# Kernel optimization log

Hardware: AMD Instinct MI355X
Metric: run time of the kernel (lower is better)

Reference implementation:

```python
import jax, jax.numpy as jnp
import numpy as np
import math

B, T, D = 4, 4096, 1024
N, L = 256, 768
H = 16
TE = 1024  # time_embed_dim


def _ln(x, g, b, eps=1e-5):
    mu = jnp.mean(x, axis=-1, keepdims=True)
    var = jnp.var(x, axis=-1, keepdims=True)
    return (x - mu) * jax.lax.rsqrt(var + eps) * g + b


def setup_inputs() -> dict:
    key = jax.random.key(0)
    ks = jax.random.split(key, 12)
    s = lambda fan_in: 1.0 / math.sqrt(fan_in)
    return {
        "x":   jax.random.normal(ks[0], (B, T, D), jnp.float32),
        "xf":  jax.random.normal(ks[1], (B, N, L), jnp.float32),
        "emb": jax.random.normal(ks[2], (B, TE), jnp.float32),
        # LayerNorm params
        "norm_g": jnp.ones((D,), jnp.float32), "norm_b": jnp.zeros((D,), jnp.float32),
        "tnorm_g": jnp.ones((L,), jnp.float32), "tnorm_b": jnp.zeros((L,), jnp.float32),
        # Q/K/V projections
        "Wq": jax.random.uniform(ks[3], (D, D), jnp.float32, -s(D), s(D)),
        "bq": jnp.zeros((D,), jnp.float32),
        "Wk": jax.random.uniform(ks[4], (L, D), jnp.float32, -s(L), s(L)),
        "bk": jnp.zeros((D,), jnp.float32),
        "Wv": jax.random.uniform(ks[5], (L, D), jnp.float32, -s(L), s(L)),
        "bv": jnp.zeros((D,), jnp.float32),
        # StylizationBlock: emb_layers Linear(TE, 2D)
        "We": jax.random.uniform(ks[6], (TE, 2 * D), jnp.float32, -s(TE), s(TE)),
        "be": jnp.zeros((2 * D,), jnp.float32),
        # StylizationBlock: inner LayerNorm + out Linear(D, D)
        "snorm_g": jnp.ones((D,), jnp.float32), "snorm_b": jnp.zeros((D,), jnp.float32),
        "Wo": jax.random.uniform(ks[7], (D, D), jnp.float32, -s(D), s(D)),
        "bo": jnp.zeros((D,), jnp.float32),
    }


def reference(x, xf, emb, norm_g, norm_b, tnorm_g, tnorm_b,
              Wq, bq, Wk, bk, Wv, bv, We, be, snorm_g, snorm_b, Wo, bo):
    dh = D // H
    xf_n = _ln(xf, tnorm_g, tnorm_b)                      # B,N,L (shared by K and V)
    q = (_ln(x, norm_g, norm_b) @ Wq + bq).reshape(B, T, H, dh)
    k = (xf_n @ Wk + bk).reshape(B, N, H, dh)
    v = (xf_n @ Wv + bv).reshape(B, N, H, dh)
    attn = jnp.einsum('bthd,bnhd->btnh', q, k) / math.sqrt(dh)
    w = jax.nn.softmax(attn, axis=2)                      # softmax over text tokens n
    y = jnp.einsum('btnh,bnhd->bthd', w, v).reshape(B, T, D)
    # StylizationBlock (AdaLN-style)
    emb_out = jax.nn.silu(emb) @ We + be                  # B, 2D
    scale, shift = jnp.split(emb_out[:, None, :], 2, axis=2)
    h = _ln(y, snorm_g, snorm_b) * (1.0 + scale) + shift
    h = jax.nn.silu(h) @ Wo + bo
    return x + h
```

## Files before the change

### kernel.cpp

```cpp
#include <hip/hip_runtime.h>

typedef unsigned short u16;
typedef short bf16x8 __attribute__((ext_vector_type(8)));
typedef float f32x4 __attribute__((ext_vector_type(4)));


__device__ __forceinline__ float b2f(u16 u) {
  union { unsigned int u; float f; } x; x.u = ((unsigned int)u) << 16; return x.f;
}
__device__ __forceinline__ u16 f2b(float f) {
  union { float f; unsigned int u; } x; x.f = f;
  unsigned int u = x.u;
  return (u16)((u + 0x7FFFu + ((u >> 16) & 1u)) >> 16);
}

#define GLOAD_LDS16(g, l)                                                      \
  __builtin_amdgcn_global_load_lds(                                            \
      (const __attribute__((address_space(1))) unsigned int*)(g),              \
      (__attribute__((address_space(3))) unsigned int*)(l), 16, 0, 0)

__global__ __launch_bounds__(256) void transpose4_k(
    const float* __restrict__ Wq, const float* __restrict__ Wk,
    const float* __restrict__ Wv, const float* __restrict__ Wo,
    u16* __restrict__ wqt, u16* __restrict__ wkt,
    u16* __restrict__ wvt, u16* __restrict__ wot,
    float* __restrict__ embo) {
  if (blockIdx.z == 0 && blockIdx.y == 0) {
    int idx = blockIdx.x * 256 + threadIdx.y * 32 + threadIdx.x;
    embo[idx] = 0.f;
  }
  const float* src; u16* dst; int R;
  switch (blockIdx.z) {
    case 0: src = Wq; dst = wqt; R = 1024; break;
    case 1: src = Wk; dst = wkt; R = 768;  break;
    case 2: src = Wv; dst = wvt; R = 768;  break;
    default: src = Wo; dst = wot; R = 1024; break;
  }
  int bx = blockIdx.x * 32, by = blockIdx.y * 32;
  if (by >= R) return;
  __shared__ float t[32][33];
  int x = threadIdx.x, y = threadIdx.y;
#pragma unroll
  for (int i = 0; i < 4; ++i)
    t[y * 4 + i][x] = src[(size_t)(by + y * 4 + i) * 1024 + bx + x];
  __syncthreads();
#pragma unroll
  for (int i = 0; i < 4; ++i)
    dst[(size_t)(bx + y * 4 + i) * R + by + x] = f2b(t[x][y * 4 + i]);
}

__global__ __launch_bounds__(256) void ln_k(const float* __restrict__ in,
                                            const float* __restrict__ g,
                                            const float* __restrict__ bta,
                                            u16* __restrict__ out, int C) {
  int row = blockIdx.x, tid = threadIdx.x;
  const float* p = in + (size_t)row * C;
  int i0 = tid * 4;
  bool act = i0 < C;
  float v0 = 0.f, v1 = 0.f, v2 = 0.f, v3 = 0.f;
  if (act) {
    float4 u = *(const float4*)(p + i0);
    v0 = u.x; v1 = u.y; v2 = u.z; v3 = u.w;
  }
  float s = v0 + v1 + v2 + v3;
  float q = v0 * v0 + v1 * v1 + v2 * v2 + v3 * v3;
  __shared__ float red[8];
#pragma unroll
  for (int m = 32; m; m >>= 1) { s += __shfl_xor(s, m); q += __shfl_xor(q, m); }
  if ((tid & 63) == 0) { red[tid >> 6] = s; red[4 + (tid >> 6)] = q; }
  __syncthreads();
  s = red[0] + red[1] + red[2] + red[3];
  q = red[4] + red[5] + red[6] + red[7];
  float invC = 1.0f / (float)C;
  float mu = s * invC;
  float rs = rsqrtf(q * invC - mu * mu + 1e-5f);
  if (act) {
    float4 ug = *(const float4*)(g + i0);
    float4 ub = *(const float4*)(bta + i0);
    ushort4 o;
    o.x = f2b((v0 - mu) * rs * ug.x + ub.x);
    o.y = f2b((v1 - mu) * rs * ug.y + ub.y);
    o.z = f2b((v2 - mu) * rs * ug.z + ub.z);
    o.w = f2b((v3 - mu) * rs * ug.w + ub.w);
    *(ushort4*)(out + (size_t)row * C + i0) = o;
  }
}

__global__ __launch_bounds__(256) void style_k(const u16* __restrict__ y,
                                               const float* __restrict__ g,
                                               const float* __restrict__ bta,
                                               const float* __restrict__ embo,
                                               u16* __restrict__ out) {
  int row = blockIdx.x, tid = threadIdx.x;
  int b = row >> 12;
  const u16* p = y + (size_t)row * 1024;
  int i0 = tid * 4;
  ushort4 u = *(const ushort4*)(p + i0);
  float v0 = b2f(u.x), v1 = b2f(u.y), v2 = b2f(u.z), v3 = b2f(u.w);
  float s = v0 + v1 + v2 + v3;
  float q = v0 * v0 + v1 * v1 + v2 * v2 + v3 * v3;
  __shared__ float red[8];
#pragma unroll
  for (int m = 32; m; m >>= 1) { s += __shfl_xor(s, m); q += __shfl_xor(q, m); }
  if ((tid & 63) == 0) { red[tid >> 6] = s; red[4 + (tid >> 6)] = q; }
  __syncthreads();
  s = red[0] + red[1] + red[2] + red[3];
  q = red[4] + red[5] + red[6] + red[7];
  const float invC = 1.0f / 1024.0f;
  float mu = s * invC;
  float rs = rsqrtf(q * invC - mu * mu + 1e-5f);
  float4 ug = *(const float4*)(g + i0);
  float4 ub = *(const float4*)(bta + i0);
  float4 sc = *(const float4*)(embo + b * 2048 + i0);
  float4 sh = *(const float4*)(embo + b * 2048 + 1024 + i0);
  float h0 = ((v0 - mu) * rs * ug.x + ub.x) * (1.0f + sc.x) + sh.x;
  float h1 = ((v1 - mu) * rs * ug.y + ub.y) * (1.0f + sc.y) + sh.y;
  float h2 = ((v2 - mu) * rs * ug.z + ub.z) * (1.0f + sc.z) + sh.z;
  float h3 = ((v3 - mu) * rs * ug.w + ub.w) * (1.0f + sc.w) + sh.w;
  ushort4 o;
  o.x = f2b(h0 / (1.0f + __expf(-h0)));
  o.y = f2b(h1 / (1.0f + __expf(-h1)));
  o.z = f2b(h2 / (1.0f + __expf(-h2)));
  o.w = f2b(h3 / (1.0f + __expf(-h3)));
  *(ushort4*)(out + (size_t)row * 1024 + i0) = o;
}

__global__ __launch_bounds__(256) void emb_k(const float* __restrict__ emb,
                                             const float* __restrict__ We,
                                             const float* __restrict__ be,
                                             float* __restrict__ embo) {
  int b = blockIdx.y, tid = threadIdx.x;
  int j = blockIdx.x * 256 + tid;
  int i0 = blockIdx.z * 128;
  __shared__ float se[128];
  if (tid < 128) {
    float v = emb[b * 1024 + i0 + tid];
    se[tid] = v / (1.0f + __expf(-v));
  }
  __syncthreads();
  float acc = (blockIdx.z == 0) ? be[j] : 0.f;
#pragma unroll 8
  for (int i = 0; i < 128; ++i) acc += se[i] * We[(size_t)(i0 + i) * 2048 + j];
  atomicAdd(&embo[b * 2048 + j], acc);
}

__global__ __launch_bounds__(256) void gemm_bt_k(const u16* __restrict__ A,
                                                 const u16* __restrict__ Bt,
                                                 const float* __restrict__ bias,
                                                 const float* __restrict__ res,
                                                 u16* __restrict__ Cb,
                                                 float* __restrict__ Cf,
                                                 int M, int Nn, int K, int mode) {
  __shared__ __align__(16) short As[128 * 64];
  __shared__ __align__(16) short Bs[128 * 64];
  int tid = threadIdx.x;
  int m0 = blockIdx.x * 128, n0 = blockIdx.y * 128;
  int wave = tid >> 6, lane = tid & 63;
  int l16 = lane & 15, quad = lane >> 4;
  int wm = (wave >> 1) * 64, wn = (wave & 1) * 64;

  f32x4 acc[4][4];
#pragma unroll
  for (int i = 0; i < 4; ++i)
#pragma unroll
    for (int j = 0; j < 4; ++j)
#pragma unroll
      for (int r = 0; r < 4; ++r) acc[i][j][r] = 0.f;

  for (int kt = 0; kt < K; kt += 64) {
#pragma unroll
    for (int p = 0; p < 4; ++p) {
      int c = p * 256 + tid;
      int r = c >> 3;
      int cd = ((c & 7) ^ (r & 7)) * 8;
      int lb = (p * 256 + wave * 64) * 8;
      GLOAD_LDS16(A + (size_t)(m0 + r) * K + kt + cd, As + lb);
      GLOAD_LDS16(Bt + (size_t)(n0 + r) * K + kt + cd, Bs + lb);
    }
    __syncthreads();
#pragma unroll
    for (int ks = 0; ks < 2; ++ks) {
      int swz = ((ks * 4 + quad) ^ (l16 & 7)) * 8;
      bf16x8 af[4], bfr[4];
#pragma unroll
      for (int i = 0; i < 4; ++i)
        af[i] = *(const bf16x8*)&As[(wm + i * 16 + l16) * 64 + swz];
#pragma unroll
      for (int j = 0; j < 4; ++j)
        bfr[j] = *(const bf16x8*)&Bs[(wn + j * 16 + l16) * 64 + swz];
#pragma unroll
      for (int i = 0; i < 4; ++i)
#pragma unroll
        for (int j = 0; j < 4; ++j)
          acc[i][j] = __builtin_amdgcn_mfma_f32_16x16x32_bf16(af[i], bfr[j], acc[i][j], 0, 0, 0);
    }
    __syncthreads();
  }

#pragma unroll
  for (int j = 0; j < 4; ++j) {
    int col = n0 + wn + j * 16 + l16;
    float bv = bias[col];
#pragma unroll
    for (int i = 0; i < 4; ++i) {
      int row0 = m0 + wm + i * 16 + quad * 4;
#pragma unroll
      for (int r = 0; r < 4; ++r) {
        int row = row0 + r;
        float v = acc[i][j][r] + bv;
        if (mode == 2) {
          Cf[(size_t)row * Nn + col] = v + res[(size_t)row * Nn + col];
        } else if (mode == 1) {
          Cb[((size_t)((row >> 8) * 1024 + col)) * 256 + (row & 255)] = f2b(v);
        } else {
          Cb[(size_t)row * Nn + col] = f2b(v);
        }
      }
    }
  }
}

__global__ __launch_bounds__(512, 4) void gemm256_k(const u16* __restrict__ A,
                                                    const u16* __restrict__ Bt,
                                                    const float* __restrict__ bias,
                                                    const float* __restrict__ res,
                                                    u16* __restrict__ Cb,
                                                    float* __restrict__ Cf,
                                                    int M, int Nn, int K, int mode) {
  __shared__ __align__(16) short smem[36864];
  short* AsB = smem;
  short* BsB = smem + 12288;
  int tid = threadIdx.x;
  int m0 = blockIdx.x * 128, n0 = blockIdx.y * 256;
  int wave = tid >> 6, lane = tid & 63;
  int l16 = lane & 15, quad = lane >> 4;
  int wm = (wave >> 2) * 64;
  int wn = (wave & 3) * 64;

  size_t offA;
  {
    int r = tid >> 2;
    int cg = (tid & 3) ^ ((r >> 1) & 3);
    offA = (size_t)(m0 + r) * K + cg * 8;
  }
  int ldsA = tid * 8;
  size_t offB[2];
  int ldsB[2];
#pragma unroll
  for (int p = 0; p < 2; ++p) {
    int c = p * 512 + tid;
    int r = c >> 2;
    int cg = (c & 3) ^ ((r >> 1) & 3);
    offB[p] = (size_t)(n0 + r) * K + cg * 8;
    ldsB[p] = c * 8;
  }

  int aoff[4], boff[4];
#pragma unroll
  for (int mi = 0; mi < 4; ++mi) {
    int R = wm + mi * 16 + l16;
    aoff[mi] = R * 32 + ((quad ^ ((R >> 1) & 3)) * 8);
  }
#pragma unroll
  for (int ni = 0; ni < 4; ++ni) {
    int R = wn + ni * 16 + l16;
    boff[ni] = R * 32 + ((quad ^ ((R >> 1) & 3)) * 8);
  }

  f32x4 acc[4][4];
#pragma unroll
  for (int i = 0; i < 4; ++i)
#pragma unroll
    for (int j = 0; j < 4; ++j)
#pragma unroll
      for (int r = 0; r < 4; ++r) acc[i][j][r] = 0.f;

#define STAGE(tt, bufc)                                                        \
  do {                                                                         \
    int kt_ = (tt) * 32;                                                       \
    GLOAD_LDS16(A + offA + kt_, AsB + (bufc) * 4096 + ldsA);                   \
    GLOAD_LDS16(Bt + offB[0] + kt_, BsB + (bufc) * 8192 + ldsB[0]);            \
    GLOAD_LDS16(Bt + offB[1] + kt_, BsB + (bufc) * 8192 + ldsB[1]);            \
  } while (0)

#define COMPUTE(curc)                                                          \
  do {                                                                         \
    const short* as_ = AsB + (curc) * 4096;                                    \
    const short* bs_ = BsB + (curc) * 8192;                                    \
    bf16x8 af[4], bfv[4];                                                      \
    _Pragma("unroll") for (int mi = 0; mi < 4; ++mi)                           \
        af[mi] = *(const bf16x8*)&as_[aoff[mi]];                               \
    _Pragma("unroll") for (int ni = 0; ni < 4; ++ni)                           \
        bfv[ni] = *(const bf16x8*)&bs_[boff[ni]];                              \
    __builtin_amdgcn_s_setprio(1);                                             \
    _Pragma("unroll") for (int mi = 0; mi < 4; ++mi)                           \
      _Pragma("unroll") for (int ni = 0; ni < 4; ++ni)                         \
        acc[mi][ni] = __builtin_amdgcn_mfma_f32_16x16x32_bf16(                 \
            af[mi], bfv[ni], acc[mi][ni], 0, 0, 0);                            \
    __builtin_amdgcn_s_setprio(0);                                             \
  } while (0)

  const int NT = K >> 5;
  STAGE(0, 0);
  STAGE(1, 1);

  int cur = 0;
  for (int t = 0; t < NT - 1; ++t) {
    asm volatile("s_waitcnt vmcnt(3)" ::: "memory");
    __builtin_amdgcn_s_barrier();
    asm volatile("" ::: "memory");
    if (t + 2 < NT) {
      int nb = cur + 2; if (nb >= 3) nb -= 3;
      STAGE(t + 2, nb);
    }
    COMPUTE(cur);
    cur = (cur == 2) ? 0 : cur + 1;
  }
  asm volatile("s_waitcnt vmcnt(0)" ::: "memory");
  __builtin_amdgcn_s_barrier();
  asm volatile("" ::: "memory");
  COMPUTE(cur);
#undef COMPUTE
#undef STAGE

  float* eps = (float*)smem;
  float bv[4];
#pragma unroll
  for (int ni = 0; ni < 4; ++ni) bv[ni] = bias[n0 + wn + ni * 16 + l16];

#pragma unroll
  for (int half = 0; half < 2; ++half) {
    __syncthreads();
    if ((wave >> 2) == half) {
#pragma unroll
      for (int mi = 0; mi < 4; ++mi) {
#pragma unroll
        for (int ni = 0; ni < 4; ++ni) {
          int col = wn + ni * 16 + l16;
#pragma unroll
          for (int r = 0; r < 4; ++r) {
            int row = mi * 16 + quad * 4 + r;
            eps[row * 256 + (col ^ (((row >> 2) & 3) << 3))] =
                acc[mi][ni][r] + bv[ni];
          }
        }
      }
    }
    __syncthreads();
#pragma unroll
    for (int p = 0; p < 8; ++p) {
      int row = wave * 8 + p;
      int grow = m0 + half * 64 + row;
      int colb = (lane * 4) ^ (((row >> 2) & 3) << 3);
      f32x4 v = *(const f32x4*)&eps[row * 256 + colb];
      if (mode == 2) {
        float4 rv = ((const float4*)&res[(size_t)grow * Nn + n0])[lane];
        float4 o;
        o.x = v[0] + rv.x; o.y = v[1] + rv.y;
        o.z = v[2] + rv.z; o.w = v[3] + rv.w;
        ((float4*)&Cf[(size_t)grow * Nn + n0])[lane] = o;
      } else {
        ushort4 o;
        o.x = f2b(v[0]); o.y = f2b(v[1]); o.z = f2b(v[2]); o.w = f2b(v[3]);
        ((ushort4*)&Cb[(size_t)grow * Nn + n0])[lane] = o;
      }
    }
  }
}

__global__ __launch_bounds__(256) void attn_k(const u16* __restrict__ Q,
                                              const u16* __restrict__ Kt,
                                              const u16* __restrict__ VT,
                                              u16* __restrict__ Y) {
  __shared__ __align__(16) short KsPs[256 * 64];
  __shared__ __align__(16) short Vt[64 * 256];
  int tid = threadIdx.x;
  int t0 = blockIdx.x * 64, h = blockIdx.y, b = blockIdx.z;
  int wave = tid >> 6, lane = tid & 63;
  int l16 = lane & 15, quad = lane >> 4;
  int wb = wave * 16;

#pragma unroll
  for (int p = 0; p < 8; ++p) {
    int c = tid + p * 256;
    int n = c >> 3, cd = c & 7;
    *(int4*)&KsPs[n * 64 + ((cd ^ (n & 7)) * 8)] =
        *(const int4*)(Kt + ((size_t)(b * 256 + n)) * 1024 + h * 64 + cd * 8);
  }
#pragma unroll
  for (int p = 0; p < 8; ++p) {
    int c = tid + p * 256;
    int d = c >> 5, ch = c & 31;
    *(int4*)&Vt[d * 256 + ((ch ^ (d & 7)) * 8)] =
        *(const int4*)(VT + ((size_t)(b * 1024 + h * 64 + d)) * 256 + ch * 8);
  }
  const u16* qrow = Q + ((size_t)(b * 4096 + t0 + wb + l16)) * 1024 + h * 64;
  bf16x8 qf0 = *(const bf16x8*)(qrow + quad * 8);
  bf16x8 qf1 = *(const bf16x8*)(qrow + 32 + quad * 8);
  __syncthreads();

  f32x4 sa[16];
#pragma unroll
  for (int mt = 0; mt < 16; ++mt)
#pragma unroll
    for (int r = 0; r < 4; ++r) sa[mt][r] = 0.f;
#pragma unroll
  for (int ks = 0; ks < 2; ++ks) {
    bf16x8 qb = ks ? qf1 : qf0;
#pragma unroll
    for (int mt = 0; mt < 16; ++mt) {
      int n = mt * 16 + l16;
      bf16x8 kf = *(const bf16x8*)&KsPs[n * 64 + (((ks * 4 + quad) ^ (n & 7)) * 8)];
      sa[mt] = __builtin_amdgcn_mfma_f32_16x16x32_bf16(kf, qb, sa[mt], 0, 0, 0);
    }
  }
  __syncthreads();

  const float CLG = 0.18033688011112042f;
  float mx = -3.0e38f;
#pragma unroll
  for (int mt = 0; mt < 16; ++mt)
#pragma unroll
    for (int r = 0; r < 4; ++r) mx = fmaxf(mx, sa[mt][r]);
  mx = fmaxf(mx, __shfl_xor(mx, 16));
  mx = fmaxf(mx, __shfl_xor(mx, 32));
  float mxc = mx * CLG;
  float sum = 0.f;
#pragma unroll
  for (int mt = 0; mt < 16; ++mt)
#pragma unroll
    for (int r = 0; r < 4; ++r) {
      float e = __builtin_exp2f(sa[mt][r] * CLG - mxc);
      sa[mt][r] = e;
      sum += e;
    }
  sum += __shfl_xor(sum, 16);
  sum += __shfl_xor(sum, 32);
  float rsc = 1.0f / sum;

  {
    int prow = wb + l16;
    short* pb = &KsPs[prow * 256 + (quad & 1) * 4];
    int q2 = quad >> 1, swz = l16 & 7;
#pragma unroll
    for (int mt = 0; mt < 16; ++mt) {
      float a0 = sa[mt][0], a1 = sa[mt][1], a2 = sa[mt][2], a3 = sa[mt][3];
      unsigned plo, phi;
      asm("v_cvt_pk_bf16_f32 %0, %1, %2" : "=v"(plo) : "v"(a0), "v"(a1));
      asm("v_cvt_pk_bf16_f32 %0, %1, %2" : "=v"(phi) : "v"(a2), "v"(a3));
      uint2 pk; pk.x = plo; pk.y = phi;
      *(uint2*)(pb + (((2 * mt + q2) ^ swz) * 8)) = pk;
    }
  }
  __syncthreads();

  f32x4 ya[4];
#pragma unroll
  for (int j = 0; j < 4; ++j)
#pragma unroll
    for (int r = 0; r < 4; ++r) ya[j][r] = 0.f;
  int m = wb + l16;
#pragma unroll
  for (int kk = 0; kk < 8; ++kk) {
    bf16x8 af = *(const bf16x8*)&KsPs[m * 256 + (((kk * 4 + quad) ^ (m & 7)) * 8)];
#pragma unroll
    for (int j = 0; j < 4; ++j) {
      int d = j * 16 + l16;
      bf16x8 bfr = *(const bf16x8*)&Vt[d * 256 + (((kk * 4 + quad) ^ (d & 7)) * 8)];
      ya[j] = __builtin_amdgcn_mfma_f32_16x16x32_bf16(af, bfr, ya[j], 0, 0, 0);
    }
  }
  float rscv[4];
#pragma unroll
  for (int r = 0; r < 4; ++r) rscv[r] = __shfl(rsc, quad * 4 + r);
#pragma unroll
  for (int j = 0; j < 4; ++j)
#pragma unroll
    for (int r = 0; r < 4; ++r)
      Y[((size_t)(b * 4096 + t0 + wb + quad * 4 + r)) * 1024 + h * 64 + j * 16 + l16] =
          f2b(ya[j][r] * rscv[r]);
}

extern "C" void kernel_launch(void* const* d_in, const int* in_sizes, int n_in,
                              void* d_out, int out_size, void* d_ws, size_t ws_size,
                              hipStream_t stream) {
  const float* x       = (const float*)d_in[0];
  const float* xf      = (const float*)d_in[1];
  const float* emb     = (const float*)d_in[2];
  const float* norm_g  = (const float*)d_in[3];
  const float* norm_b  = (const float*)d_in[4];
  const float* tnorm_g = (const float*)d_in[5];
  const float* tnorm_b = (const float*)d_in[6];
  const float* Wq      = (const float*)d_in[7];
  const float* bq      = (const float*)d_in[8];
  const float* Wk      = (const float*)d_in[9];
  const float* bk      = (const float*)d_in[10];
  const float* Wv      = (const float*)d_in[11];
  const float* bv      = (const float*)d_in[12];
  const float* We      = (const float*)d_in[13];
  const float* be      = (const float*)d_in[14];
  const float* snorm_g = (const float*)d_in[15];
  const float* snorm_b = (const float*)d_in[16];
  const float* Wo      = (const float*)d_in[17];
  const float* bo      = (const float*)d_in[18];

  const size_t MB = 1024 * 1024;
  char* dout = (char*)d_out;
  u16* qbuf = (u16*)(dout);
  u16* wqt  = (u16*)(dout + 32 * MB);
  u16* wkt  = (u16*)(dout + 34 * MB);
  u16* wvt  = (u16*)(dout + 36 * MB);
  float* out = (float*)d_out;

  char* ws = (char*)d_ws;
  u16* big1 = (u16*)(ws);
  u16* xfn  = (u16*)(ws + 32 * MB);
  u16* kws  = (u16*)(ws + 33 * MB + 512 * 1024);
  u16* vtws = (u16*)(ws + 35 * MB + 512 * 1024);
  u16* wot  = (u16*)(ws + 37 * MB + 512 * 1024);
  float* embo = (float*)(ws + 39 * MB + 512 * 1024);

  transpose4_k<<<dim3(32, 32, 4), dim3(32, 8), 0, stream>>>(
      Wq, Wk, Wv, Wo, wqt, wkt, wvt, wot, embo);

  ln_k<<<16384, 256, 0, stream>>>(x, norm_g, norm_b, big1, 1024);
  ln_k<<<1024, 256, 0, stream>>>(xf, tnorm_g, tnorm_b, xfn, 768);

  gemm256_k<<<dim3(128, 4), 512, 0, stream>>>(big1, wqt, bq, nullptr, qbuf, nullptr, 16384, 1024, 1024, 0);
  gemm_bt_k<<<dim3(8, 8), 256, 0, stream>>>(xfn, wkt, bk, nullptr, kws, nullptr, 1024, 1024, 768, 0);
  gemm_bt_k<<<dim3(8, 8), 256, 0, stream>>>(xfn, wvt, bv, nullptr, vtws, nullptr, 1024, 1024, 768, 1);

  emb_k<<<dim3(8, 4, 8), 256, 0, stream>>>(emb, We, be, embo);

  attn_k<<<dim3(64, 16, 4), 256, 0, stream>>>(qbuf, kws, vtws, big1);

  style_k<<<16384, 256, 0, stream>>>(big1, snorm_g, snorm_b, embo, big1);

  gemm256_k<<<dim3(128, 4), 512, 0, stream>>>(big1, wot, bo, x, nullptr, out, 16384, 1024, 1024, 2);
}
```

Before: 371.5 us.

## Merge K/V projections into one launch; stream K via LDS DMA, read V from global

The separate K and V projection GEMM launches become one kernel launch, with blockIdx.z choosing the weight, bias and output layout. In the attention kernel, K is now staged into LDS with global_load_lds direct copies, and the XOR swizzle is applied on the global source address. V is no longer staged in LDS and is read straight from global memory inside the PV MFMA loop. This saves a launch, halves the LDS footprint per block (which may raise occupancy) and removes a staging pass, but the PV loop now depends on global/L2 latency for V.

```diff
diff --git a/kernel.cpp b/kernel.cpp
--- a/kernel.cpp
+++ b/kernel.cpp
@@ -144,13 +144,16 @@
   atomicAdd(&embo[b * 2048 + j], acc);
 }
 
-__global__ __launch_bounds__(256) void gemm_bt_k(const u16* __restrict__ A,
-                                                 const u16* __restrict__ Bt,
-                                                 const float* __restrict__ bias,
-                                                 const float* __restrict__ res,
-                                                 u16* __restrict__ Cb,
-                                                 float* __restrict__ Cf,
-                                                 int M, int Nn, int K, int mode) {
+__global__ __launch_bounds__(256) void kvproj_k(const u16* __restrict__ A,
+                                                const u16* __restrict__ WkT,
+                                                const u16* __restrict__ WvT,
+                                                const float* __restrict__ bk_,
+                                                const float* __restrict__ bv_,
+                                                u16* __restrict__ Ck,
+                                                u16* __restrict__ Cv) {
+  const int K = 768, Nn = 1024;
+  const u16* Bt = blockIdx.z ? WvT : WkT;
+  const float* bias = blockIdx.z ? bv_ : bk_;
   __shared__ __align__(16) short As[128 * 64];
   __shared__ __align__(16) short Bs[128 * 64];
   int tid = threadIdx.x;
@@ -208,12 +211,10 @@
       for (int r = 0; r < 4; ++r) {
         int row = row0 + r;
         float v = acc[i][j][r] + bv;
-        if (mode == 2) {
-          Cf[(size_t)row * Nn + col] = v + res[(size_t)row * Nn + col];
-        } else if (mode == 1) {
-          Cb[((size_t)((row >> 8) * 1024 + col)) * 256 + (row & 255)] = f2b(v);
+        if (blockIdx.z) {
+          Cv[((size_t)((row >> 8) * 1024 + col)) * 256 + (row & 255)] = f2b(v);
         } else {
-          Cb[(size_t)row * Nn + col] = f2b(v);
+          Ck[(size_t)row * Nn + col] = f2b(v);
         }
       }
     }
@@ -373,7 +374,6 @@
                                               const u16* __restrict__ VT,
                                               u16* __restrict__ Y) {
   __shared__ __align__(16) short KsPs[256 * 64];
-  __shared__ __align__(16) short Vt[64 * 256];
   int tid = threadIdx.x;
   int t0 = blockIdx.x * 64, h = blockIdx.y, b = blockIdx.z;
   int wave = tid >> 6, lane = tid & 63;
@@ -382,21 +382,15 @@
 
 #pragma unroll
   for (int p = 0; p < 8; ++p) {
-    int c = tid + p * 256;
-    int n = c >> 3, cd = c & 7;
-    *(int4*)&KsPs[n * 64 + ((cd ^ (n & 7)) * 8)] =
-        *(const int4*)(Kt + ((size_t)(b * 256 + n)) * 1024 + h * 64 + cd * 8);
-  }
-#pragma unroll
-  for (int p = 0; p < 8; ++p) {
-    int c = tid + p * 256;
-    int d = c >> 5, ch = c & 31;
-    *(int4*)&Vt[d * 256 + ((ch ^ (d & 7)) * 8)] =
-        *(const int4*)(VT + ((size_t)(b * 1024 + h * 64 + d)) * 256 + ch * 8);
+    int c = p * 256 + tid;
+    int n = c >> 3, s = c & 7;
+    GLOAD_LDS16(Kt + ((size_t)(b * 256 + n)) * 1024 + h * 64 + ((s ^ (n & 7)) * 8),
+                KsPs + (p * 256 + wave * 64) * 8);
   }
   const u16* qrow = Q + ((size_t)(b * 4096 + t0 + wb + l16)) * 1024 + h * 64;
   bf16x8 qf0 = *(const bf16x8*)(qrow + quad * 8);
   bf16x8 qf1 = *(const bf16x8*)(qrow + 32 + quad * 8);
+  asm volatile("s_waitcnt vmcnt(0)" ::: "memory");
   __syncthreads();
 
   f32x4 sa[16];
@@ -454,6 +448,7 @@
   }
   __syncthreads();
 
+  const u16* vb = VT + ((size_t)(b * 1024 + h * 64)) * 256;
   f32x4 ya[4];
 #pragma unroll
   for (int j = 0; j < 4; ++j)
@@ -465,8 +460,7 @@
     bf16x8 af = *(const bf16x8*)&KsPs[m * 256 + (((kk * 4 + quad) ^ (m & 7)) * 8)];
 #pragma unroll
     for (int j = 0; j < 4; ++j) {
-      int d = j * 16 + l16;
-      bf16x8 bfr = *(const bf16x8*)&Vt[d * 256 + (((kk * 4 + quad) ^ (d & 7)) * 8)];
+      bf16x8 bfr = *(const bf16x8*)(vb + (size_t)(j * 16 + l16) * 256 + kk * 32 + quad * 8);
       ya[j] = __builtin_amdgcn_mfma_f32_16x16x32_bf16(af, bfr, ya[j], 0, 0, 0);
     }
   }
@@ -527,8 +521,7 @@
   ln_k<<<1024, 256, 0, stream>>>(xf, tnorm_g, tnorm_b, xfn, 768);
 
   gemm256_k<<<dim3(128, 4), 512, 0, stream>>>(big1, wqt, bq, nullptr, qbuf, nullptr, 16384, 1024, 1024, 0);
-  gemm_bt_k<<<dim3(8, 8), 256, 0, stream>>>(xfn, wkt, bk, nullptr, kws, nullptr, 1024, 1024, 768, 0);
-  gemm_bt_k<<<dim3(8, 8), 256, 0, stream>>>(xfn, wvt, bv, nullptr, vtws, nullptr, 1024, 1024, 768, 1);
+  kvproj_k<<<dim3(8, 8, 2), 256, 0, stream>>>(xfn, wkt, wvt, bk, bv, kws, vtws);
 
   emb_k<<<dim3(8, 4, 8), 256, 0, stream>>>(emb, We, be, embo);
 
```

Result: slower. 386.8 us (+4.1%).
